# Optimization experiments

Measured on AMD Instinct MI355X. Metric: run time of the kernel, lower is better.

The kernel has to match this reference:

```python
import jax, jax.numpy as jnp
import numpy as np

ORDER = 2
C_IN = 32   # per-hop feature dim d
C_OUT = 64


def setup_inputs() -> dict:
    key = jax.random.key(0)
    k = jax.random.split(key, 6)
    b, num_n, num_m, d, t = 2, 512, 256, C_IN, 128
    feat_context = jax.random.normal(k[0], (b, num_n, d, t), dtype=jnp.float32)
    feat_target = jax.random.normal(k[1], (b, num_m, d, t), dtype=jnp.float32)
    adj = jax.random.uniform(k[2], (b, ORDER, num_m, num_n), dtype=jnp.float32)
    missing_mask_context = jax.random.randint(k[3], (b, t, num_n), 0, 2).astype(jnp.float32)
    c_cat = (ORDER + 1) * d  # 96
    W_mlp = jax.random.normal(k[4], (C_OUT, c_cat), dtype=jnp.float32) / np.sqrt(c_cat)
    b_mlp = jax.random.normal(k[5], (C_OUT,), dtype=jnp.float32) * 0.01
    return {"feat_context": feat_context, "feat_target": feat_target, "adj": adj,
            "missing_mask_context": missing_mask_context, "W_mlp": W_mlp, "b_mlp": b_mlp}


def _aggregate(fc_btnd, ft_btmd, adj_bmn, mask_btn):
    # mask out missing context nodes, per (batch, time)
    a = adj_bmn[:, None, :, :] * (1.0 - mask_btn[:, :, None, :])   # [b,t,m,n]
    norm = a / (jnp.sum(a, axis=-1, keepdims=True) + 1.0)          # [b,t,m,n]
    # residual + adjacency-weighted neighbor sum (batched matmul instead of [b,t,m,n,d] blow-up)
    agg = ft_btmd + jnp.einsum('btmn,btnd->btmd', norm, fc_btnd)   # [b,t,m,d]
    return agg


def reference(feat_context, feat_target, adj, missing_mask_context, W_mlp, b_mlp):
    # feat_context: [b,n,d,t], feat_target: [b,m,d,t], adj: [b,k,m,n], mask: [b,t,n]
    fc = jnp.transpose(feat_context, (0, 3, 1, 2))  # [b,t,n,d]
    ft = jnp.transpose(feat_target, (0, 3, 1, 2))   # [b,t,m,d]
    outs = [feat_target]
    for i in range(ORDER):
        agg = _aggregate(fc, ft, adj[:, i], missing_mask_context)      # [b,t,m,d]
        outs.append(jnp.transpose(agg, (0, 2, 3, 1)))                  # [b,m,d,t]
    out = jnp.concatenate(outs, axis=2)  # [b,m,(order+1)*d,t]
    # 1x1 conv over the feature channel dim + ReLU (dropout is identity at eval)
    y = jnp.einsum('bmct,oc->bmot', out, W_mlp) + b_mlp[None, None, :, None]
    return jax.nn.relu(y)  # [b,m,c_out,t]
```

## Files before the change

kernel.cpp:

```cpp
#include <hip/hip_runtime.h>
#include <cstdint>
#include <cstddef>


using shortx8 = __attribute__((ext_vector_type(8))) short;
using floatx4 = __attribute__((ext_vector_type(4))) float;

__device__ __forceinline__ float b2f(unsigned short u) {
    union { unsigned int i; float f; } v; v.i = ((unsigned int)u) << 16; return v.f;
}
__device__ __forceinline__ unsigned short f2b(float f) {
    union { float f; unsigned int i; } v; v.f = f;
    unsigned int x = v.i;
    return (unsigned short)((x + 0x7FFFu + ((x >> 16) & 1u)) >> 16);
}
__device__ __forceinline__ void gl_lds16(const unsigned short* g, unsigned short* l) {
    __builtin_amdgcn_global_load_lds(
        (const __attribute__((address_space(1))) unsigned int*)g,
        (__attribute__((address_space(3))) unsigned int*)l, 16, 0, 0);
}

__global__ void k_prep(const float* __restrict__ fc, const float* __restrict__ mask,
                       const float* __restrict__ adj,
                       unsigned short* __restrict__ gt, unsigned short* __restrict__ adjb) {
    const int tid = threadIdx.x;
    __shared__ float wls[32][33];
    __shared__ unsigned short tls[32][34];

    if (blockIdx.x < 4224) {
        const int r_ = blockIdx.x;
        const int jb = r_ % 132;
        const int rem = r_ / 132;
        const int nb = rem & 15, b = rem >> 4;
        const int n0 = nb * 32;
        const int r = tid >> 3, c4 = (tid & 7) * 4;
        if (jb >= 128) {
            const int t0 = (jb - 128) * 32;
            float4 mv = *(const float4*)(mask + ((size_t)b * 128 + t0 + r) * 512 + n0 + c4);
            ushort4 o;
            o.x = f2b(1.f - mv.x); o.y = f2b(1.f - mv.y);
            o.z = f2b(1.f - mv.z); o.w = f2b(1.f - mv.w);
            *(ushort4*)(gt + ((size_t)b * 4224 + 4096 + t0 + r) * 512 + n0 + c4) = o;
            return;
        }
        const int j0 = jb * 32;
        const int t0 = j0 & 127;
        {
            float4 mv = *(const float4*)(mask + ((size_t)b * 128 + t0 + r) * 512 + n0 + c4);
            wls[r][c4 + 0] = 1.f - mv.x; wls[r][c4 + 1] = 1.f - mv.y;
            wls[r][c4 + 2] = 1.f - mv.z; wls[r][c4 + 3] = 1.f - mv.w;
        }
        float4 fv = *(const float4*)(fc + ((size_t)b * 512 + n0 + r) * 4096 + j0 + c4);
        __syncthreads();
        tls[c4 + 0][r] = f2b(fv.x * wls[c4 + 0][r]);
        tls[c4 + 1][r] = f2b(fv.y * wls[c4 + 1][r]);
        tls[c4 + 2][r] = f2b(fv.z * wls[c4 + 2][r]);
        tls[c4 + 3][r] = f2b(fv.w * wls[c4 + 3][r]);
        __syncthreads();
        ushort4 o;
        o.x = tls[r][c4 + 0]; o.y = tls[r][c4 + 1];
        o.z = tls[r][c4 + 2]; o.w = tls[r][c4 + 3];
        *(ushort4*)(gt + ((size_t)b * 4224 + j0 + r) * 512 + n0 + c4) = o;
    } else {
        int i4 = ((blockIdx.x - 4224) * 256 + tid) * 4;
        float4 v = *(const float4*)(adj + i4);
        ushort4 o;
        o.x = f2b(v.x); o.y = f2b(v.y); o.z = f2b(v.z); o.w = f2b(v.w);
        *(ushort4*)(adjb + i4) = o;
    }
}

__launch_bounds__(256, 3)
__global__ void k_gemm(const unsigned short* __restrict__ adjb,
                       const unsigned short* __restrict__ gt,
                       unsigned short* __restrict__ ut,
                       unsigned short* __restrict__ sbuf) {
    const int jt = blockIdx.x, mt = blockIdx.y, bi = blockIdx.z;
    const int b = bi >> 1;
    const int tid = threadIdx.x;
    const int wave = tid >> 6, lane = tid & 63;
    const int l15 = lane & 15, quad = lane >> 4;
    const int wm = wave & 1, wj = wave >> 1;

    __shared__ __align__(16) unsigned short Al[2][64 * 64];
    __shared__ __align__(16) unsigned short Bl[2][128 * 64];

    const int srow = lane >> 3;
    const int skq  = (lane & 7) * 8;
    const unsigned short* Ag = adjb + ((size_t)bi * 256 + mt * 64) * 512;
    const unsigned short* Bgb = gt + (size_t)b * 4224 * 512;

    #define STAGE(buf, k0)                                                        \
        _Pragma("unroll")                                                         \
        for (int rr = 0; rr < 2; ++rr) {                                          \
            const int ch = wave * 2 + rr;                      \
            const int row = ch * 8 + srow;                                        \
            gl_lds16(Ag + (size_t)row * 512 + (k0) + skq, &Al[buf][ch * 512]);    \
        }                                                                         \
        _Pragma("unroll")                                                         \
        for (int rr = 0; rr < 4; ++rr) {                                          \
            const int ch = wave * 4 + rr;                     \
            const int row = ch * 8 + srow;                                        \
            const int jrow = (jt < 32) ? ((row & 31) * 128 + jt * 4 + (row >> 5)) \
                                       : (4096 + row);                            \
            gl_lds16(Bgb + (size_t)jrow * 512 + (k0) + skq, &Bl[buf][ch * 512]);  \
        }

    floatx4 acc[2][4];
    #pragma unroll
    for (int i = 0; i < 2; ++i)
        #pragma unroll
        for (int j = 0; j < 4; ++j) acc[i][j] = (floatx4){0.f, 0.f, 0.f, 0.f};

    STAGE(0, 0)
    int cur = 0;
    for (int it = 0; it < 8; ++it) {
        __syncthreads();
        if (it < 7) { STAGE(cur ^ 1, (it + 1) * 64) }
        #pragma unroll
        for (int ks = 0; ks < 2; ++ks) {
            shortx8 af[2], bf[4];
            #pragma unroll
            for (int i = 0; i < 2; ++i)
                af[i] = *(const shortx8*)&Al[cur][(wm * 32 + i * 16 + l15) * 64 + ks * 32 + quad * 8];
            #pragma unroll
            for (int j = 0; j < 4; ++j)
                bf[j] = *(const shortx8*)&Bl[cur][(wj * 64 + j * 16 + l15) * 64 + ks * 32 + quad * 8];
            #pragma unroll
            for (int i = 0; i < 2; ++i)
                #pragma unroll
                for (int j = 0; j < 4; ++j)
                    acc[i][j] = __builtin_amdgcn_mfma_f32_16x16x32_bf16(af[i], bf[j], acc[i][j], 0, 0, 0);
        }
        cur ^= 1;
    }
    #undef STAGE

    if (jt < 32) {
        #pragma unroll
        for (int i = 0; i < 2; ++i)
            #pragma unroll
            for (int jj = 0; jj < 4; ++jj) {
                const int d_   = (jj & 1) * 16 + l15;
                const int tloc = wj * 2 + (jj >> 1);
                const int t_   = jt * 4 + tloc;
                #pragma unroll
                for (int reg = 0; reg < 4; ++reg) {
                    const int m_ = mt * 64 + wm * 32 + i * 16 + quad * 4 + reg;
                    ut[(((size_t)bi * 256 + m_) * 128 + t_) * 32 + d_] = f2b(acc[i][jj][reg]);
                }
            }
    } else {
        #pragma unroll
        for (int i = 0; i < 2; ++i)
            #pragma unroll
            for (int jj = 0; jj < 4; ++jj) {
                const int t_ = wj * 64 + jj * 16 + l15;
                #pragma unroll
                for (int reg = 0; reg < 4; ++reg) {
                    const int m_ = mt * 64 + wm * 32 + i * 16 + quad * 4 + reg;
                    sbuf[((size_t)bi * 256 + m_) * 128 + t_] = f2b(acc[i][jj][reg]);
                }
            }
    }
}

__launch_bounds__(256)
__global__ void k_mlp(const float* __restrict__ ft, const unsigned short* __restrict__ ut,
                      const unsigned short* __restrict__ sbuf, const float* __restrict__ W,
                      const float* __restrict__ bias, float* __restrict__ y) {
    const int m = blockIdx.x, b = blockIdx.y, tz = blockIdx.z;
    const int tbase = tz * 64;
    const int tid = threadIdx.x;
    const int wave = tid >> 6, lane = tid & 63;
    const int l15 = lane & 15, quad = lane >> 4;

    __shared__ unsigned short ftt[64 * 32];

    {
        const int d = tid >> 3, t0 = (tid & 7) * 8;
        const float* src = ft + ((size_t)(b * 256 + m) * 32 + d) * 128 + tbase + t0;
        float4 v0 = *(const float4*)(src);
        float4 v1 = *(const float4*)(src + 4);
        float fv[8] = { v0.x, v0.y, v0.z, v0.w, v1.x, v1.y, v1.z, v1.w };
        #pragma unroll
        for (int i = 0; i < 8; ++i) ftt[(t0 + i) * 32 + d] = f2b(fv[i]);
    }

    const int o_ = wave * 16 + l15;
    shortx8 aw, a2, a3;
    {
        const float* wp = W + (size_t)o_ * 96 + quad * 8;
        float4 p0 = *(const float4*)(wp),      p1 = *(const float4*)(wp + 4);
        float4 q0 = *(const float4*)(wp + 32), q1 = *(const float4*)(wp + 36);
        float4 r0_ = *(const float4*)(wp + 64), r1_ = *(const float4*)(wp + 68);
        float w1[8] = { p0.x, p0.y, p0.z, p0.w, p1.x, p1.y, p1.z, p1.w };
        float w2[8] = { q0.x, q0.y, q0.z, q0.w, q1.x, q1.y, q1.z, q1.w };
        float w3[8] = { r0_.x, r0_.y, r0_.z, r0_.w, r1_.x, r1_.y, r1_.z, r1_.w };
        #pragma unroll
        for (int j = 0; j < 8; ++j) {
            aw[j] = (short)f2b(w1[j] + w2[j] + w3[j]);
            a2[j] = (short)f2b(w2[j]);
            a3[j] = (short)f2b(w3[j]);
        }
    }
    float bv[4];
    #pragma unroll
    for (int r = 0; r < 4; ++r) bv[r] = bias[wave * 16 + quad * 4 + r];

    const unsigned short* u0 = ut + ((size_t)((2 * b + 0) * 256 + m) * 128 + tbase) * 32;
    const unsigned short* u1 = ut + ((size_t)((2 * b + 1) * 256 + m) * 128 + tbase) * 32;
    const unsigned short* s0 = sbuf + ((size_t)(2 * b + 0) * 256 + m) * 128 + tbase;
    const unsigned short* s1 = sbuf + ((size_t)(2 * b + 1) * 256 + m) * 128 + tbase;
    float* yp = y + ((size_t)(b * 256 + m) * 64) * 128 + tbase;

    __syncthreads();

    #pragma unroll
    for (int tt = 0; tt < 4; ++tt) {
        const int t = tt * 16 + l15;
        shortx8 bf = *(const shortx8*)&ftt[t * 32 + quad * 8];
        shortx8 b0 = *(const shortx8*)(u0 + (size_t)t * 32 + quad * 8);
        shortx8 b1 = *(const shortx8*)(u1 + (size_t)t * 32 + quad * 8);
        floatx4 z = {0.f, 0.f, 0.f, 0.f};
        floatx4 cw = __builtin_amdgcn_mfma_f32_16x16x32_bf16(aw, bf, z, 0, 0, 0);
        floatx4 c2 = __builtin_amdgcn_mfma_f32_16x16x32_bf16(a2, b0, z, 0, 0, 0);
        floatx4 c3 = __builtin_amdgcn_mfma_f32_16x16x32_bf16(a3, b1, z, 0, 0, 0);
        float r0 = 1.f / (b2f(s0[t]) + 1.f);
        float r1 = 1.f / (b2f(s1[t]) + 1.f);
        #pragma unroll
        for (int r = 0; r < 4; ++r) {
            const int o = wave * 16 + quad * 4 + r;
            float v = cw[r] + r0 * c2[r] + r1 * c3[r] + bv[r];
            yp[(size_t)o * 128 + t] = v > 0.f ? v : 0.f;
        }
    }
}

extern "C" void kernel_launch(void* const* d_in, const int* in_sizes, int n_in,
                              void* d_out, int out_size, void* d_ws, size_t ws_size,
                              hipStream_t stream) {
    const float* fc   = (const float*)d_in[0];
    const float* ft   = (const float*)d_in[1];
    const float* adj  = (const float*)d_in[2];
    const float* mask = (const float*)d_in[3];
    const float* W    = (const float*)d_in[4];
    const float* bias = (const float*)d_in[5];
    float* y = (float*)d_out;

    unsigned short* gt   = (unsigned short*)d_ws;
    unsigned short* adjb = gt   + (size_t)2 * 4224 * 512;
    unsigned short* ut   = adjb + (size_t)4 * 256 * 512;
    unsigned short* sbuf = ut   + (size_t)4 * 256 * 128 * 32;

    k_prep<<<4736, 256, 0, stream>>>(fc, mask, adj, gt, adjb);
    k_gemm<<<dim3(33, 4, 4), 256, 0, stream>>>(adjb, gt, ut, sbuf);
    k_mlp <<<dim3(256, 2, 2), 256, 0, stream>>>(ft, ut, sbuf, W, bias, y);
}
```

Measured before the change: 108.7 us.

## Fuse adjacency GEMM with MLP epilogue and move ft/W conversion into prep

Merges the aggregation GEMM and the 1x1-conv MLP into one kernel. Each block computes both hop orders for 32 target nodes and 4 time steps, then keeps the aggregated features and row sums in LDS and applies the MLP, bias and ReLU directly. This removes the ut/sbuf global round trip and one kernel launch. The prep kernel now also converts ft and the folded weights to bf16, and LDS accesses use XOR swizzling to avoid bank conflicts. The trade-offs are more LDS per block, lower occupancy (launch bound 2), redundant B-tile loads shared across both orders, and scattered 4-byte output stores.

```diff
diff --git a/kernel.cpp b/kernel.cpp
--- a/kernel.cpp
+++ b/kernel.cpp
@@ -6,9 +6,6 @@
 using shortx8 = __attribute__((ext_vector_type(8))) short;
 using floatx4 = __attribute__((ext_vector_type(4))) float;
 
-__device__ __forceinline__ float b2f(unsigned short u) {
-    union { unsigned int i; float f; } v; v.i = ((unsigned int)u) << 16; return v.f;
-}
 __device__ __forceinline__ unsigned short f2b(float f) {
     union { float f; unsigned int i; } v; v.f = f;
     unsigned int x = v.i;
@@ -21,16 +18,18 @@
 }
 
 __global__ void k_prep(const float* __restrict__ fc, const float* __restrict__ mask,
-                       const float* __restrict__ adj,
-                       unsigned short* __restrict__ gt, unsigned short* __restrict__ adjb) {
+                       const float* __restrict__ adj, const float* __restrict__ ft,
+                       const float* __restrict__ W,
+                       unsigned short* __restrict__ gt, unsigned short* __restrict__ adjb,
+                       unsigned short* __restrict__ ftb, unsigned short* __restrict__ wb) {
     const int tid = threadIdx.x;
     __shared__ float wls[32][33];
     __shared__ unsigned short tls[32][34];
-
-    if (blockIdx.x < 4224) {
-        const int r_ = blockIdx.x;
-        const int jb = r_ % 132;
-        const int rem = r_ / 132;
+    const int x = blockIdx.x;
+
+    if (x < 4224) {
+        const int jb = x % 132;
+        const int rem = x / 132;
         const int nb = rem & 15, b = rem >> 4;
         const int n0 = nb * 32;
         const int r = tid >> 3, c4 = (tid & 7) * 4;
@@ -61,178 +60,196 @@
         o.x = tls[r][c4 + 0]; o.y = tls[r][c4 + 1];
         o.z = tls[r][c4 + 2]; o.w = tls[r][c4 + 3];
         *(ushort4*)(gt + ((size_t)b * 4224 + j0 + r) * 512 + n0 + c4) = o;
-    } else {
-        int i4 = ((blockIdx.x - 4224) * 256 + tid) * 4;
+    } else if (x < 4736) {
+        int i4 = ((x - 4224) * 256 + tid) * 4;
         float4 v = *(const float4*)(adj + i4);
         ushort4 o;
         o.x = f2b(v.x); o.y = f2b(v.y); o.z = f2b(v.z); o.w = f2b(v.w);
         *(ushort4*)(adjb + i4) = o;
-    }
-}
-
-__launch_bounds__(256, 3)
-__global__ void k_gemm(const unsigned short* __restrict__ adjb,
-                       const unsigned short* __restrict__ gt,
-                       unsigned short* __restrict__ ut,
-                       unsigned short* __restrict__ sbuf) {
-    const int jt = blockIdx.x, mt = blockIdx.y, bi = blockIdx.z;
-    const int b = bi >> 1;
+    } else if (x < 6784) {
+        const int fb = x - 4736;
+        const int b = fb >> 10, rem = fb & 1023;
+        const int m = rem >> 2, tb = rem & 3;
+        const int r = tid >> 3, c4 = (tid & 7) * 4;
+        float4 fv = *(const float4*)(ft + (((size_t)(b * 256 + m)) * 32 + r) * 128 + tb * 32 + c4);
+        tls[c4 + 0][r] = f2b(fv.x); tls[c4 + 1][r] = f2b(fv.y);
+        tls[c4 + 2][r] = f2b(fv.z); tls[c4 + 3][r] = f2b(fv.w);
+        __syncthreads();
+        ushort4 o;
+        o.x = tls[r][c4 + 0]; o.y = tls[r][c4 + 1];
+        o.z = tls[r][c4 + 2]; o.w = tls[r][c4 + 3];
+        *(ushort4*)(ftb + (((size_t)(b * 256 + m)) * 128 + tb * 32 + r) * 32 + c4) = o;
+    } else {
+        if (tid < 64) {
+            for (int c = 0; c < 32; ++c) {
+                float w1 = W[tid * 96 + c];
+                float w2 = W[tid * 96 + 32 + c];
+                float w3 = W[tid * 96 + 64 + c];
+                wb[tid * 96 + c]      = f2b(w1 + w2 + w3);
+                wb[tid * 96 + 32 + c] = f2b(w2);
+                wb[tid * 96 + 64 + c] = f2b(w3);
+            }
+        }
+    }
+}
+
+__launch_bounds__(256, 2)
+__global__ void k_fused(const unsigned short* __restrict__ adjb,
+                        const unsigned short* __restrict__ gt,
+                        const unsigned short* __restrict__ ftb,
+                        const unsigned short* __restrict__ wb,
+                        const float* __restrict__ bias, float* __restrict__ y) {
+    const int jt = blockIdx.x, mt = blockIdx.y, b = blockIdx.z;
+    const int t0 = jt * 4, m0 = mt * 32;
     const int tid = threadIdx.x;
     const int wave = tid >> 6, lane = tid & 63;
     const int l15 = lane & 15, quad = lane >> 4;
-    const int wm = wave & 1, wj = wave >> 1;
-
-    __shared__ __align__(16) unsigned short Al[2][64 * 64];
-    __shared__ __align__(16) unsigned short Bl[2][128 * 64];
-
+    const int wo = wave & 1, wj = wave >> 1;
     const int srow = lane >> 3;
-    const int skq  = (lane & 7) * 8;
-    const unsigned short* Ag = adjb + ((size_t)bi * 256 + mt * 64) * 512;
-    const unsigned short* Bgb = gt + (size_t)b * 4224 * 512;
-
-    #define STAGE(buf, k0)                                                        \
-        _Pragma("unroll")                                                         \
-        for (int rr = 0; rr < 2; ++rr) {                                          \
-            const int ch = wave * 2 + rr;                      \
-            const int row = ch * 8 + srow;                                        \
-            gl_lds16(Ag + (size_t)row * 512 + (k0) + skq, &Al[buf][ch * 512]);    \
-        }                                                                         \
-        _Pragma("unroll")                                                         \
-        for (int rr = 0; rr < 4; ++rr) {                                          \
-            const int ch = wave * 4 + rr;                     \
-            const int row = ch * 8 + srow;                                        \
-            const int jrow = (jt < 32) ? ((row & 31) * 128 + jt * 4 + (row >> 5)) \
-                                       : (4096 + row);                            \
-            gl_lds16(Bgb + (size_t)jrow * 512 + (k0) + skq, &Bl[buf][ch * 512]);  \
-        }
-
-    floatx4 acc[2][4];
-    #pragma unroll
-    for (int i = 0; i < 2; ++i)
+    const int ksw = (((lane & 7) ^ srow) * 8);
+
+    __shared__ __align__(16) unsigned short Al[2][2][32 * 64];
+    __shared__ __align__(16) unsigned short Bl[2][144 * 64];
+    __shared__ __align__(16) unsigned short Fl[128 * 32];
+    __shared__ __align__(16) unsigned short Ul[2][128 * 32];
+    __shared__ float Rl[2 * 128];
+
+    const unsigned short* gtb = gt + (size_t)b * 4224 * 512;
+
+    #define STAGE(buf, k0)                                                            \
+        _Pragma("unroll")                                                             \
+        for (int aa = 0; aa < 2; ++aa) {                                              \
+            const int a = wave * 2 + aa;                                    \
+            const int ord = a >> 2, ch = a & 3;                                       \
+            const int row = ch * 8 + srow;                                            \
+            gl_lds16(adjb + ((size_t)((b * 2 + ord) * 256 + m0 + row)) * 512          \
+                          + (k0) + ksw,                                               \
+                     &Al[buf][ord][ch * 512]);                                        \
+        }                                                                             \
+        _Pragma("unroll")                                                             \
+        for (int rr = 0; rr < 4; ++rr) {                                              \
+            const int ch = wave * 4 + rr;                                  \
+            const int row = ch * 8 + srow;                                            \
+            const int jrow = (row & 31) * 128 + t0 + (row >> 5);                      \
+            gl_lds16(gtb + (size_t)jrow * 512 + (k0) + ksw, &Bl[buf][ch * 512]);      \
+        }                                                                             \
+        if (wave < 2)                                                                 \
+            gl_lds16(gtb + (size_t)(4096 + t0 + (srow & 3)) * 512 + (k0) + ksw,       \
+                     &Bl[buf][128 * 64 + wave * 512]);
+
+    floatx4 acc[2][4], sacc[2];
+    #pragma unroll
+    for (int i = 0; i < 2; ++i) {
+        sacc[i] = (floatx4){0.f, 0.f, 0.f, 0.f};
         #pragma unroll
         for (int j = 0; j < 4; ++j) acc[i][j] = (floatx4){0.f, 0.f, 0.f, 0.f};
+    }
 
     STAGE(0, 0)
+    #pragma unroll
+    for (int cc = 0; cc < 2; ++cc) {
+        const int c = wave * 2 + cc;
+        const int col = c * 16 + (lane >> 2), qs = lane & 3;
+        gl_lds16(ftb + (((size_t)(b * 256 + m0 + (col >> 2))) * 128 + t0 + (col & 3)) * 32
+                     + ((qs ^ (col & 3)) * 8),
+                 &Fl[c * 512]);
+    }
+
     int cur = 0;
     for (int it = 0; it < 8; ++it) {
         __syncthreads();
         if (it < 7) { STAGE(cur ^ 1, (it + 1) * 64) }
         #pragma unroll
         for (int ks = 0; ks < 2; ++ks) {
+            const int swz = (((ks * 4 + quad) ^ (l15 & 7)) << 4);
             shortx8 af[2], bf[4];
             #pragma unroll
             for (int i = 0; i < 2; ++i)
-                af[i] = *(const shortx8*)&Al[cur][(wm * 32 + i * 16 + l15) * 64 + ks * 32 + quad * 8];
-            #pragma unroll
-            for (int j = 0; j < 4; ++j)
-                bf[j] = *(const shortx8*)&Bl[cur][(wj * 64 + j * 16 + l15) * 64 + ks * 32 + quad * 8];
+                af[i] = *(const shortx8*)((const char*)&Al[cur][wo][0]
+                                          + (i * 16 + l15) * 128 + swz);
+            #pragma unroll
+            for (int jj = 0; jj < 4; ++jj)
+                bf[jj] = *(const shortx8*)((const char*)&Bl[cur][0]
+                                           + (wj * 64 + jj * 16 + l15) * 128 + swz);
             #pragma unroll
             for (int i = 0; i < 2; ++i)
                 #pragma unroll
-                for (int j = 0; j < 4; ++j)
-                    acc[i][j] = __builtin_amdgcn_mfma_f32_16x16x32_bf16(af[i], bf[j], acc[i][j], 0, 0, 0);
+                for (int jj = 0; jj < 4; ++jj)
+                    acc[i][jj] = __builtin_amdgcn_mfma_f32_16x16x32_bf16(af[i], bf[jj],
+                                                                         acc[i][jj], 0, 0, 0);
+            if (wj == 0) {
+                shortx8 sf = *(const shortx8*)((const char*)&Bl[cur][0]
+                                               + (128 + l15) * 128 + swz);
+                #pragma unroll
+                for (int i = 0; i < 2; ++i)
+                    sacc[i] = __builtin_amdgcn_mfma_f32_16x16x32_bf16(af[i], sf,
+                                                                      sacc[i], 0, 0, 0);
+            }
         }
         cur ^= 1;
     }
     #undef STAGE
 
-    if (jt < 32) {
+    shortx8 aws[4], aw2[4], aw3[4];
+    float4 bv[4];
+    #pragma unroll
+    for (int of = 0; of < 4; ++of) {
+        const unsigned short* wrow = wb + (size_t)(of * 16 + l15) * 96;
+        aws[of] = *(const shortx8*)(wrow + quad * 8);
+        aw2[of] = *(const shortx8*)(wrow + 32 + quad * 8);
+        aw3[of] = *(const shortx8*)(wrow + 64 + quad * 8);
+        bv[of]  = *(const float4*)(bias + of * 16 + quad * 4);
+    }
+
+    #pragma unroll
+    for (int i = 0; i < 2; ++i)
+        #pragma unroll
+        for (int jj = 0; jj < 4; ++jj) {
+            const int d = (jj & 1) * 16 + l15;
+            const int tl = wj * 2 + (jj >> 1);
+            #pragma unroll
+            for (int reg = 0; reg < 4; ++reg) {
+                const int m_loc = i * 16 + quad * 4 + reg;
+                const int col = m_loc * 4 + tl;
+                const int byteoff = (wo * 128 + col) * 64
+                                  + ((((d >> 3) ^ (col & 3))) << 4) + (d & 7) * 2;
+                *(unsigned short*)((char*)&Ul[0][0] + byteoff) = f2b(acc[i][jj][reg]);
+            }
+        }
+    if (wj == 0 && l15 < 4) {
         #pragma unroll
         for (int i = 0; i < 2; ++i)
             #pragma unroll
-            for (int jj = 0; jj < 4; ++jj) {
-                const int d_   = (jj & 1) * 16 + l15;
-                const int tloc = wj * 2 + (jj >> 1);
-                const int t_   = jt * 4 + tloc;
-                #pragma unroll
-                for (int reg = 0; reg < 4; ++reg) {
-                    const int m_ = mt * 64 + wm * 32 + i * 16 + quad * 4 + reg;
-                    ut[(((size_t)bi * 256 + m_) * 128 + t_) * 32 + d_] = f2b(acc[i][jj][reg]);
-                }
-            }
-    } else {
-        #pragma unroll
-        for (int i = 0; i < 2; ++i)
-            #pragma unroll
-            for (int jj = 0; jj < 4; ++jj) {
-                const int t_ = wj * 64 + jj * 16 + l15;
-                #pragma unroll
-                for (int reg = 0; reg < 4; ++reg) {
-                    const int m_ = mt * 64 + wm * 32 + i * 16 + quad * 4 + reg;
-                    sbuf[((size_t)bi * 256 + m_) * 128 + t_] = f2b(acc[i][jj][reg]);
-                }
-            }
-    }
-}
-
-__launch_bounds__(256)
-__global__ void k_mlp(const float* __restrict__ ft, const unsigned short* __restrict__ ut,
-                      const unsigned short* __restrict__ sbuf, const float* __restrict__ W,
-                      const float* __restrict__ bias, float* __restrict__ y) {
-    const int m = blockIdx.x, b = blockIdx.y, tz = blockIdx.z;
-    const int tbase = tz * 64;
-    const int tid = threadIdx.x;
-    const int wave = tid >> 6, lane = tid & 63;
-    const int l15 = lane & 15, quad = lane >> 4;
-
-    __shared__ unsigned short ftt[64 * 32];
-
-    {
-        const int d = tid >> 3, t0 = (tid & 7) * 8;
-        const float* src = ft + ((size_t)(b * 256 + m) * 32 + d) * 128 + tbase + t0;
-        float4 v0 = *(const float4*)(src);
-        float4 v1 = *(const float4*)(src + 4);
-        float fv[8] = { v0.x, v0.y, v0.z, v0.w, v1.x, v1.y, v1.z, v1.w };
-        #pragma unroll
-        for (int i = 0; i < 8; ++i) ftt[(t0 + i) * 32 + d] = f2b(fv[i]);
-    }
-
-    const int o_ = wave * 16 + l15;
-    shortx8 aw, a2, a3;
-    {
-        const float* wp = W + (size_t)o_ * 96 + quad * 8;
-        float4 p0 = *(const float4*)(wp),      p1 = *(const float4*)(wp + 4);
-        float4 q0 = *(const float4*)(wp + 32), q1 = *(const float4*)(wp + 36);
-        float4 r0_ = *(const float4*)(wp + 64), r1_ = *(const float4*)(wp + 68);
-        float w1[8] = { p0.x, p0.y, p0.z, p0.w, p1.x, p1.y, p1.z, p1.w };
-        float w2[8] = { q0.x, q0.y, q0.z, q0.w, q1.x, q1.y, q1.z, q1.w };
-        float w3[8] = { r0_.x, r0_.y, r0_.z, r0_.w, r1_.x, r1_.y, r1_.z, r1_.w };
-        #pragma unroll
-        for (int j = 0; j < 8; ++j) {
-            aw[j] = (short)f2b(w1[j] + w2[j] + w3[j]);
-            a2[j] = (short)f2b(w2[j]);
-            a3[j] = (short)f2b(w3[j]);
-        }
-    }
-    float bv[4];
-    #pragma unroll
-    for (int r = 0; r < 4; ++r) bv[r] = bias[wave * 16 + quad * 4 + r];
-
-    const unsigned short* u0 = ut + ((size_t)((2 * b + 0) * 256 + m) * 128 + tbase) * 32;
-    const unsigned short* u1 = ut + ((size_t)((2 * b + 1) * 256 + m) * 128 + tbase) * 32;
-    const unsigned short* s0 = sbuf + ((size_t)(2 * b + 0) * 256 + m) * 128 + tbase;
-    const unsigned short* s1 = sbuf + ((size_t)(2 * b + 1) * 256 + m) * 128 + tbase;
-    float* yp = y + ((size_t)(b * 256 + m) * 64) * 128 + tbase;
-
+            for (int reg = 0; reg < 4; ++reg) {
+                const int m_loc = i * 16 + quad * 4 + reg;
+                Rl[wo * 128 + m_loc * 4 + l15] = 1.f / (sacc[i][reg] + 1.f);
+            }
+    }
     __syncthreads();
 
     #pragma unroll
-    for (int tt = 0; tt < 4; ++tt) {
-        const int t = tt * 16 + l15;
-        shortx8 bf = *(const shortx8*)&ftt[t * 32 + quad * 8];
-        shortx8 b0 = *(const shortx8*)(u0 + (size_t)t * 32 + quad * 8);
-        shortx8 b1 = *(const shortx8*)(u1 + (size_t)t * 32 + quad * 8);
-        floatx4 z = {0.f, 0.f, 0.f, 0.f};
-        floatx4 cw = __builtin_amdgcn_mfma_f32_16x16x32_bf16(aw, bf, z, 0, 0, 0);
-        floatx4 c2 = __builtin_amdgcn_mfma_f32_16x16x32_bf16(a2, b0, z, 0, 0, 0);
-        floatx4 c3 = __builtin_amdgcn_mfma_f32_16x16x32_bf16(a3, b1, z, 0, 0, 0);
-        float r0 = 1.f / (b2f(s0[t]) + 1.f);
-        float r1 = 1.f / (b2f(s1[t]) + 1.f);
-        #pragma unroll
-        for (int r = 0; r < 4; ++r) {
-            const int o = wave * 16 + quad * 4 + r;
-            float v = cw[r] + r0 * c2[r] + r1 * c3[r] + bv[r];
-            yp[(size_t)o * 128 + t] = v > 0.f ? v : 0.f;
+    for (int cc = 0; cc < 2; ++cc) {
+        const int cf = wave * 2 + cc;
+        const int col = cf * 16 + l15;
+        const float r0 = Rl[col], r1 = Rl[128 + col];
+        const int sw = ((quad ^ (col & 3)) << 4);
+        shortx8 bfF = *(const shortx8*)((const char*)&Fl[0] + col * 64 + sw);
+        shortx8 b0  = *(const shortx8*)((const char*)&Ul[0][0] + col * 64 + sw);
+        shortx8 b1  = *(const shortx8*)((const char*)&Ul[0][0] + (128 + col) * 64 + sw);
+        float* yp = y + ((size_t)(b * 256 + m0 + (col >> 2))) * 8192 + t0 + (col & 3);
+        #pragma unroll
+        for (int of = 0; of < 4; ++of) {
+            floatx4 z = {0.f, 0.f, 0.f, 0.f};
+            floatx4 cw = __builtin_amdgcn_mfma_f32_16x16x32_bf16(aws[of], bfF, z, 0, 0, 0);
+            floatx4 c2 = __builtin_amdgcn_mfma_f32_16x16x32_bf16(aw2[of], b0, z, 0, 0, 0);
+            floatx4 c3 = __builtin_amdgcn_mfma_f32_16x16x32_bf16(aw3[of], b1, z, 0, 0, 0);
+            #pragma unroll
+            for (int reg = 0; reg < 4; ++reg) {
+                const int o = of * 16 + quad * 4 + reg;
+                float v = cw[reg] + r0 * c2[reg] + r1 * c3[reg]
+                        + ((const float*)&bv[of])[reg];
+                yp[(size_t)o * 128] = v > 0.f ? v : 0.f;
+            }
         }
     }
 }
@@ -250,10 +267,9 @@
 
     unsigned short* gt   = (unsigned short*)d_ws;
     unsigned short* adjb = gt   + (size_t)2 * 4224 * 512;
-    unsigned short* ut   = adjb + (size_t)4 * 256 * 512;
-    unsigned short* sbuf = ut   + (size_t)4 * 256 * 128 * 32;
-
-    k_prep<<<4736, 256, 0, stream>>>(fc, mask, adj, gt, adjb);
-    k_gemm<<<dim3(33, 4, 4), 256, 0, stream>>>(adjb, gt, ut, sbuf);
-    k_mlp <<<dim3(256, 2, 2), 256, 0, stream>>>(ft, ut, sbuf, W, bias, y);
-}
+    unsigned short* ftb  = adjb + (size_t)4 * 256 * 512;
+    unsigned short* wb   = ftb  + (size_t)2 * 256 * 128 * 32;
+
+    k_prep <<<6785, 256, 0, stream>>>(fc, mask, adj, ft, W, gt, adjb, ftb, wb);
+    k_fused<<<dim3(32, 8, 2), 256, 0, stream>>>(adjb, gt, ftb, wb, bias, y);
+}
```

After: 110.5 us. No clear change (+1.7%).
